# Kernel optimization log

Measured on AMD Instinct MI355X. Metric: run time of the kernel, lower is better.

The kernel has to match this reference:

```python
import jax, jax.numpy as jnp
import numpy as np

N, L, S, D, H, DK = 4, 2048, 2048, 1024, 16, 64


def setup_inputs() -> dict:
    key = jax.random.key(0)
    kq, kk, kv, kwq, kwo = jax.random.split(key, 5)
    Q = jax.random.normal(kq, (N, L, D), dtype=jnp.float32)
    K = jax.random.normal(kk, (N, S, D), dtype=jnp.float32)
    V = jax.random.normal(kv, (N, S, D), dtype=jnp.float32)
    # per-head query projection weights (the source reuses Lq for K and V too)
    Wq = jax.random.normal(kwq, (H, DK, D), dtype=jnp.float32) * (D ** -0.5)
    # output projection Lo: Linear(h*dv -> Dv), weight shape (out, in)
    Wo = jax.random.normal(kwo, (D, H * DK), dtype=jnp.float32) * ((H * DK) ** -0.5)
    return {"Q": Q, "K": K, "V": V, "Wq": Wq, "Wo": Wo}


def reference(Q, K, V, Wq, Wo):
    dk = Wq.shape[1]
    # Faithful to source: ALL of q, k, v are projected with the Lq weights.
    q = jnp.einsum('nld,hkd->hnlk', Q, Wq)   # (H,N,L,dk)
    k = jnp.einsum('nsd,hkd->hnsk', K, Wq)   # (H,N,S,dk)
    v = jnp.einsum('nsd,hkd->hnsk', V, Wq)   # (H,N,S,dk)
    scale = jnp.asarray(dk, Q.dtype) ** 0.5
    scores = jnp.einsum('hnlk,hnsk->hnls', q, k) / scale  # (H,N,L,S)
    # Faithful to F.softmax(dot) with no dim on a 3D tensor: torch picks dim=0
    # (the batch axis N); here that is axis=1 of the head-stacked (H,N,L,S).
    attn = jax.nn.softmax(scores, axis=1)
    heads = jnp.einsum('hnls,hnsk->hnlk', attn, v)        # (H,N,L,dk)
    # concat heads along last dim -> (N,L,H*dk)
    heads = jnp.transpose(heads, (1, 2, 0, 3)).reshape(Q.shape[0], Q.shape[1], -1)
    return heads @ Wo.T  # (N,L,Dv)
```

## Files before the change

kernel.cpp:

```cpp
#include <hip/hip_runtime.h>
#include <hip/hip_bf16.h>

typedef __attribute__((ext_vector_type(8))) short short8;
typedef __attribute__((ext_vector_type(4))) short short4v;
typedef __attribute__((ext_vector_type(4))) float float4v;

#define DEVI static __device__ __forceinline__

#if __has_builtin(__builtin_amdgcn_exp2f)
#define EXP2(x) __builtin_amdgcn_exp2f(x)
#else
#define EXP2(x) exp2f(x)
#endif

DEVI unsigned short f2bf(float f) {
  unsigned int u = __builtin_bit_cast(unsigned int, f);
  u += 0x7fffu + ((u >> 16) & 1u);
  return (unsigned short)(u >> 16);
}

DEVI short8 pack8(float4v a, float4v b) {
  struct P4 { __hip_bfloat162 x, y, z, w; } t;
  t.x = __float22bfloat162_rn(make_float2(a[0], a[1]));
  t.y = __float22bfloat162_rn(make_float2(a[2], a[3]));
  t.z = __float22bfloat162_rn(make_float2(b[0], b[1]));
  t.w = __float22bfloat162_rn(make_float2(b[2], b[3]));
  short8 r;
  __builtin_memcpy(&r, &t, 16);
  return r;
}

DEVI short4v pack4(float a, float b, float c, float d) {
  struct P2 { __hip_bfloat162 x, y; } t;
  t.x = __float22bfloat162_rn(make_float2(a, b));
  t.y = __float22bfloat162_rn(make_float2(c, d));
  short4v r;
  __builtin_memcpy(&r, &t, 8);
  return r;
}

DEVI void gload16(const void* src, void* lds_dst) {
  __builtin_amdgcn_global_load_lds(
      (const __attribute__((address_space(1))) void*)src,
      (__attribute__((address_space(3))) void*)lds_dst, 16, 0, 0);
}

__global__ __launch_bounds__(256)
void cvt_bf16(const float* __restrict__ in, unsigned short* __restrict__ out, int n8)
{
  int i = blockIdx.x * 256 + threadIdx.x;
  if (i < n8) {
    float4v a = *(const float4v*)(in + (size_t)i * 8);
    float4v b = *(const float4v*)(in + (size_t)i * 8 + 4);
    *(short8*)(out + (size_t)i * 8) = pack8(a, b);
  }
}

template<int AF32, int CMODE>
__global__ __launch_bounds__(256, 2)
void gemm_bt128(const void* __restrict__ Ap, const unsigned short* __restrict__ Bp,
                void* __restrict__ Cp, int M, int Nc, int Kd, float oscale)
{
  constexpr int AS = AF32 ? 40 : 32;
  __shared__ alignas(16) short As[2][128 * AS];
  __shared__ alignas(16) short Bs[2][128 * 32];

  const int tid = threadIdx.x;
  const int lane = tid & 63;
  const int wid = tid >> 6;
  const int rl = lane & 15;
  const int g = lane >> 4;
  const int bm = blockIdx.x * 128;
  const int bn = blockIdx.y * 128;
  const int wm = (wid >> 1) * 64;
  const int wn = (wid & 1) * 64;
  const int srow = tid >> 1;
  const int k0 = (tid & 1) * 16;

  float4v acc[4][4];
#pragma unroll
  for (int i = 0; i < 4; ++i)
#pragma unroll
    for (int j = 0; j < 4; ++j) acc[i][j] = (float4v)(0.0f);

  const float* Af = (const float*)Ap;
  const unsigned short* Ab = (const unsigned short*)Ap;

  float4v afr[4];
  short8 ah[2];

  const int NK = Kd >> 5;

  const int grow = (tid >> 2) + 0;
  const int gchk = tid & 3;

  auto stageB = [&](int ks, int b) {
#pragma unroll
    for (int j = 0; j < 2; ++j) {
      const unsigned short* src = Bp + (size_t)(bn + grow + j * 64) * Kd + ks * 32 + gchk * 8;
      gload16(src, (char*)Bs[b] + j * 4096 + wid * 1024);
    }
  };
  auto stageA16 = [&](int ks, int b) {
#pragma unroll
    for (int j = 0; j < 2; ++j) {
      const unsigned short* src = Ab + (size_t)(bm + grow + j * 64) * Kd + ks * 32 + gchk * 8;
      gload16(src, (char*)As[b] + j * 4096 + wid * 1024);
    }
  };
  auto loadA = [&](int ks) {
    size_t base = (size_t)(bm + srow) * Kd + ks * 32 + k0;
    afr[0] = *(const float4v*)(Af + base);
    afr[1] = *(const float4v*)(Af + base + 4);
    afr[2] = *(const float4v*)(Af + base + 8);
    afr[3] = *(const float4v*)(Af + base + 12);
  };
  auto packWriteA = [&](int b) {
    ah[0] = pack8(afr[0], afr[1]);
    ah[1] = pack8(afr[2], afr[3]);
    *(short8*)(As[b] + srow * 40 + k0)     = ah[0];
    *(short8*)(As[b] + srow * 40 + k0 + 8) = ah[1];
  };

  stageB(0, 0);
  if constexpr (AF32 != 0) {
    loadA(0);
    packWriteA(0);
  } else {
    stageA16(0, 0);
  }
  __syncthreads();

  for (int ks = 0; ks < NK; ++ks) {
    const int b = ks & 1;
    if (ks + 1 < NK) {
      stageB(ks + 1, b ^ 1);
      if constexpr (AF32 != 0) loadA(ks + 1);
      else stageA16(ks + 1, b ^ 1);
    }

    short8 a8[4], b8[4];
#pragma unroll
    for (int mt = 0; mt < 4; ++mt)
      a8[mt] = *(const short8*)(As[b] + (wm + mt * 16 + rl) * AS + 8 * g);
#pragma unroll
    for (int nt = 0; nt < 4; ++nt)
      b8[nt] = *(const short8*)(Bs[b] + (wn + nt * 16 + rl) * 32 + 8 * g);
#pragma unroll
    for (int mt = 0; mt < 4; ++mt)
#pragma unroll
      for (int nt = 0; nt < 4; ++nt)
        acc[mt][nt] = __builtin_amdgcn_mfma_f32_16x16x32_bf16(a8[mt], b8[nt], acc[mt][nt], 0, 0, 0);

    if constexpr (AF32 != 0)
      if (ks + 1 < NK) packWriteA(b ^ 1);
    __syncthreads();
  }

#pragma unroll
  for (int mt = 0; mt < 4; ++mt)
#pragma unroll
    for (int nt = 0; nt < 4; ++nt) {
      const int col = bn + wn + nt * 16 + rl;
      const int row0 = bm + wm + mt * 16 + 4 * g;
      if constexpr (CMODE == 1) {
        float* C = (float*)Cp;
#pragma unroll
        for (int r = 0; r < 4; ++r)
          C[(size_t)(row0 + r) * Nc + col] = acc[mt][nt][r];
      } else if constexpr (CMODE == 0) {
        unsigned short* C = (unsigned short*)Cp;
#pragma unroll
        for (int r = 0; r < 4; ++r)
          C[(size_t)(row0 + r) * Nc + col] = f2bf(acc[mt][nt][r] * oscale);
      } else {
        unsigned short* C = (unsigned short*)Cp;
        short4v w = pack4(acc[mt][nt][0], acc[mt][nt][1], acc[mt][nt][2], acc[mt][nt][3]);
        const int u = row0 & 31;
        const int pm = (row0 & ~31) | (((u >> 2) & 3) << 3) | (((u >> 4) & 1) << 2);
        *(short4v*)(C + (size_t)col * M + pm) = w;
      }
    }
}

__global__ __launch_bounds__(512, 2)
void attn_bn(const unsigned short* __restrict__ qb,
             const unsigned short* __restrict__ kb,
             const unsigned short* __restrict__ vtb,
             unsigned short* __restrict__ hb)
{
  __shared__ alignas(128) char smem[131072];

  const int tid = threadIdx.x;
  const int lane = tid & 63;
  const int wid = tid >> 6;
  const int rl = lane & 15;
  const int g = lane >> 4;
  const int h = blockIdx.y;
  const int l0 = blockIdx.x * 128 + wid * 16;

  short8 qf[4][2];
#pragma unroll
  for (int n = 0; n < 4; ++n)
#pragma unroll
    for (int dh = 0; dh < 2; ++dh)
      qf[n][dh] = *(const short8*)(qb + (size_t)(n * 2048 + l0 + rl) * 1024 + h * 64 + dh * 32 + 8 * g);

  float4v ha[4][4];
#pragma unroll
  for (int n = 0; n < 4; ++n)
#pragma unroll
    for (int t = 0; t < 4; ++t) ha[n][t] = (float4v)(0.0f);

  const size_t koff0 = ((size_t)(wid * 2048) + (size_t)(lane >> 3)) * 1024
                     + (size_t)(h * 64) + (size_t)(((lane & 7) ^ (lane >> 3)) * 8);
  const size_t voff0 = ((size_t)(h * 64) + (size_t)(lane >> 2)) * 8192
                     + (size_t)((wid - 4) * 2048)
                     + (size_t)((((lane & 3) ^ ((lane >> 3) & 3)) * 8));

  auto stage = [&](int step, int b) {
    if (wid < 4) {
      char* kdst = smem + b * 32768 + wid * 4096;
      const unsigned short* ksrc = kb + koff0 + (size_t)step * 32 * 1024;
#pragma unroll
      for (int ii = 0; ii < 4; ++ii)
        gload16(ksrc + ii * 8192, kdst + ii * 1024);
    } else {
      char* vdst = smem + b * 32768 + 16384 + (wid - 4) * 4096;
      const unsigned short* vsrc = vtb + voff0 + (size_t)step * 32;
#pragma unroll
      for (int ii = 0; ii < 4; ++ii)
        gload16(vsrc + (size_t)ii * 16 * 8192, vdst + ii * 1024);
    }
  };

  stage(0, 0);
  stage(1, 1);
  stage(2, 2);
  asm volatile("s_waitcnt vmcnt(8)" ::: "memory");
  __builtin_amdgcn_s_barrier();

  const unsigned voffr = ((unsigned)(g ^ ((rl >> 1) & 3))) << 4;

  for (int to = 0; to < 16; ++to) {
#pragma unroll
    for (int ti = 0; ti < 4; ++ti) {
      const int t = to * 4 + ti;
      char* kbase = smem + ti * 32768;
      char* vbase = kbase + 16384;

      float4v sc[4][2];
#pragma unroll
      for (int n = 0; n < 4; ++n) {
        char* kn = kbase + n * 4096;
#pragma unroll
        for (int ss = 0; ss < 2; ++ss) {
          const int srw = ss * 16 + rl;
          const unsigned sw = ((unsigned)(srw & 7)) << 4;
          short8 kf0 = *(const short8*)(kn + srw * 128 + ((16u * (unsigned)g) ^ sw));
          short8 kf1 = *(const short8*)(kn + srw * 128 + ((64u + 16u * (unsigned)g) ^ sw));
          float4v c = (float4v)(0.0f);
          c = __builtin_amdgcn_mfma_f32_16x16x32_bf16(kf0, qf[n][0], c, 0, 0, 0);
          c = __builtin_amdgcn_mfma_f32_16x16x32_bf16(kf1, qf[n][1], c, 0, 0, 0);
          sc[n][ss] = c;
        }
      }

      float ex[4][2][4];
#pragma unroll
      for (int ss = 0; ss < 2; ++ss) {
#pragma unroll
        for (int n = 0; n < 4; ++n)
#pragma unroll
          for (int r = 0; r < 4; ++r)
            ex[n][ss][r] = EXP2(sc[n][ss][r]);
#pragma unroll
        for (int r = 0; r < 4; ++r) {
          float inv = __builtin_amdgcn_rcpf((ex[0][ss][r] + ex[1][ss][r])
                                          + (ex[2][ss][r] + ex[3][ss][r]) + 1e-30f);
          ex[0][ss][r] *= inv; ex[1][ss][r] *= inv;
          ex[2][ss][r] *= inv; ex[3][ss][r] *= inv;
        }
      }
      short8 pf8[4];
#pragma unroll
      for (int n = 0; n < 4; ++n) {
        float4v e0 = {ex[n][0][0], ex[n][0][1], ex[n][0][2], ex[n][0][3]};
        float4v e1 = {ex[n][1][0], ex[n][1][1], ex[n][1][2], ex[n][1][3]};
        pf8[n] = pack8(e0, e1);
      }

#pragma unroll
      for (int n = 0; n < 4; ++n) {
        char* vn = vbase + n * 4096;
#pragma unroll
        for (int t4 = 0; t4 < 4; ++t4) {
          short8 va = *(const short8*)(vn + (t4 * 16 + rl) * 64 + voffr);
          ha[n][t4] = __builtin_amdgcn_mfma_f32_16x16x32_bf16(va, pf8[n], ha[n][t4], 0, 0, 0);
        }
      }

      if (t + 3 < 64) stage(t + 3, (ti + 3) & 3);
      asm volatile("s_waitcnt vmcnt(8)" ::: "memory");
      __builtin_amdgcn_s_barrier();
    }
  }

#pragma unroll
  for (int n = 0; n < 4; ++n)
#pragma unroll
    for (int tt = 0; tt < 4; ++tt) {
      short4v w = pack4(ha[n][tt][0], ha[n][tt][1], ha[n][tt][2], ha[n][tt][3]);
      size_t off = (size_t)(n * 2048 + l0 + rl) * 1024 + h * 64 + tt * 16 + 4 * g;
      *(short4v*)(hb + off) = w;
    }
}

extern "C" void kernel_launch(void* const* d_in, const int* in_sizes, int n_in,
                              void* d_out, int out_size, void* d_ws, size_t ws_size,
                              hipStream_t stream)
{
  const float* Q  = (const float*)d_in[0];
  const float* K  = (const float*)d_in[1];
  const float* V  = (const float*)d_in[2];
  const float* Wq = (const float*)d_in[3];
  const float* Wo = (const float*)d_in[4];

  unsigned short* qb  = (unsigned short*)d_ws;
  unsigned short* kw  = qb + (size_t)8192 * 1024;
  unsigned short* vt  = kw + (size_t)8192 * 1024;
  unsigned short* wqb = vt + (size_t)8192 * 1024;
  unsigned short* wob = wqb + (size_t)1024 * 1024;
  unsigned short* hw  = qb;

  const float CS = 0.18033688011112042f;

  dim3 gg(64, 8), bb(256);
  cvt_bf16<<<512, 256, 0, stream>>>(Wq, wqb, 131072);
  cvt_bf16<<<512, 256, 0, stream>>>(Wo, wob, 131072);
  gemm_bt128<1, 0><<<gg, bb, 0, stream>>>(Q, wqb, qb, 8192, 1024, 1024, CS);
  gemm_bt128<1, 0><<<gg, bb, 0, stream>>>(K, wqb, kw, 8192, 1024, 1024, 1.0f);
  gemm_bt128<1, 2><<<gg, bb, 0, stream>>>(V, wqb, vt, 8192, 1024, 1024, 1.0f);
  attn_bn<<<dim3(16, 16), dim3(512), 0, stream>>>(qb, kw, vt, hw);
  gemm_bt128<0, 1><<<gg, bb, 0, stream>>>(hw, wob, (float*)d_out, 8192, 1024, 1024, 1.0f);
}
```

Baseline: 239.2 us.

## Split batch axis across wave pairs, exchanging partial softmax sums via LDS

Each wave now handles two batch slices and 32 query rows instead of all four batch slices and 16 rows. Each K and V fragment loaded from LDS is therefore reused across two query tiles, which roughly halves LDS reads per MFMA. Because the softmax runs over the batch axis, paired waves exchange their partial exponent sums through an extra 16KB LDS buffer, synchronised with an added barrier each step. The exchanged sums are rounded to bf16, which costs some accuracy, and the larger LDS footprint may limit occupancy.

After: 249.1 us. +4.2%, slower.

```diff
diff --git a/kernel.cpp b/kernel.cpp
--- a/kernel.cpp
+++ b/kernel.cpp
@@ -17,6 +17,10 @@
   unsigned int u = __builtin_bit_cast(unsigned int, f);
   u += 0x7fffu + ((u >> 16) & 1u);
   return (unsigned short)(u >> 16);
+}
+
+DEVI float bf2f(unsigned short s) {
+  return __builtin_bit_cast(float, ((unsigned)s) << 16);
 }
 
 DEVI short8 pack8(float4v a, float4v b) {
@@ -91,7 +95,7 @@
 
   const int NK = Kd >> 5;
 
-  const int grow = (tid >> 2) + 0;
+  const int grow = tid >> 2;
   const int gchk = tid & 3;
 
   auto stageB = [&](int ks, int b) {
@@ -189,7 +193,7 @@
              const unsigned short* __restrict__ vtb,
              unsigned short* __restrict__ hb)
 {
-  __shared__ alignas(128) char smem[131072];
+  __shared__ alignas(128) char smem[147456];
 
   const int tid = threadIdx.x;
   const int lane = tid & 63;
@@ -197,20 +201,28 @@
   const int rl = lane & 15;
   const int g = lane >> 4;
   const int h = blockIdx.y;
-  const int l0 = blockIdx.x * 128 + wid * 16;
-
-  short8 qf[4][2];
-#pragma unroll
-  for (int n = 0; n < 4; ++n)
-#pragma unroll
-    for (int dh = 0; dh < 2; ++dh)
-      qf[n][dh] = *(const short8*)(qb + (size_t)(n * 2048 + l0 + rl) * 1024 + h * 64 + dh * 32 + 8 * g);
-
-  float4v ha[4][4];
-#pragma unroll
-  for (int n = 0; n < 4; ++n)
-#pragma unroll
-    for (int t = 0; t < 4; ++t) ha[n][t] = (float4v)(0.0f);
+  const int lg = wid & 3;
+  const int nh = wid >> 2;
+  const int n0 = nh * 2;
+  const int l0 = blockIdx.x * 128 + lg * 32;
+
+  short8 qf[2][2][2];
+#pragma unroll
+  for (int j = 0; j < 2; ++j)
+#pragma unroll
+    for (int lt = 0; lt < 2; ++lt)
+#pragma unroll
+      for (int dh = 0; dh < 2; ++dh)
+        qf[j][lt][dh] = *(const short8*)(qb
+            + (size_t)((n0 + j) * 2048 + l0 + lt * 16 + rl) * 1024 + h * 64 + dh * 32 + 8 * g);
+
+  float4v ha[2][2][4];
+#pragma unroll
+  for (int j = 0; j < 2; ++j)
+#pragma unroll
+    for (int lt = 0; lt < 2; ++lt)
+#pragma unroll
+      for (int t = 0; t < 4; ++t) ha[j][lt][t] = (float4v)(0.0f);
 
   const size_t koff0 = ((size_t)(wid * 2048) + (size_t)(lane >> 3)) * 1024
                      + (size_t)(h * 64) + (size_t)(((lane & 7) ^ (lane >> 3)) * 8);
@@ -241,6 +253,8 @@
   __builtin_amdgcn_s_barrier();
 
   const unsigned voffr = ((unsigned)(g ^ ((rl >> 1) & 3))) << 4;
+  char* exW = smem + 131072 + wid * 2048 + lane * 32;
+  char* exR = smem + 131072 + (wid ^ 4) * 2048 + lane * 32;
 
   for (int to = 0; to < 16; ++to) {
 #pragma unroll
@@ -249,54 +263,76 @@
       char* kbase = smem + ti * 32768;
       char* vbase = kbase + 16384;
 
-      float4v sc[4][2];
-#pragma unroll
-      for (int n = 0; n < 4; ++n) {
-        char* kn = kbase + n * 4096;
+      float4v sc[2][2][2];
+#pragma unroll
+      for (int j = 0; j < 2; ++j) {
+        char* kn = kbase + (n0 + j) * 4096;
 #pragma unroll
         for (int ss = 0; ss < 2; ++ss) {
           const int srw = ss * 16 + rl;
           const unsigned sw = ((unsigned)(srw & 7)) << 4;
           short8 kf0 = *(const short8*)(kn + srw * 128 + ((16u * (unsigned)g) ^ sw));
           short8 kf1 = *(const short8*)(kn + srw * 128 + ((64u + 16u * (unsigned)g) ^ sw));
-          float4v c = (float4v)(0.0f);
-          c = __builtin_amdgcn_mfma_f32_16x16x32_bf16(kf0, qf[n][0], c, 0, 0, 0);
-          c = __builtin_amdgcn_mfma_f32_16x16x32_bf16(kf1, qf[n][1], c, 0, 0, 0);
-          sc[n][ss] = c;
-        }
-      }
-
-      float ex[4][2][4];
-#pragma unroll
-      for (int ss = 0; ss < 2; ++ss) {
-#pragma unroll
-        for (int n = 0; n < 4; ++n)
+#pragma unroll
+          for (int lt = 0; lt < 2; ++lt) {
+            float4v c = (float4v)(0.0f);
+            c = __builtin_amdgcn_mfma_f32_16x16x32_bf16(kf0, qf[j][lt][0], c, 0, 0, 0);
+            c = __builtin_amdgcn_mfma_f32_16x16x32_bf16(kf1, qf[j][lt][1], c, 0, 0, 0);
+            sc[j][lt][ss] = c;
+          }
+        }
+      }
+
+      float ex[2][2][2][4];
+      float4v ps[2][2];
+#pragma unroll
+      for (int lt = 0; lt < 2; ++lt)
+#pragma unroll
+        for (int ss = 0; ss < 2; ++ss) {
+#pragma unroll
+          for (int j = 0; j < 2; ++j)
+#pragma unroll
+            for (int r = 0; r < 4; ++r)
+              ex[j][lt][ss][r] = EXP2(sc[j][lt][ss][r]);
 #pragma unroll
           for (int r = 0; r < 4; ++r)
-            ex[n][ss][r] = EXP2(sc[n][ss][r]);
-#pragma unroll
-        for (int r = 0; r < 4; ++r) {
-          float inv = __builtin_amdgcn_rcpf((ex[0][ss][r] + ex[1][ss][r])
-                                          + (ex[2][ss][r] + ex[3][ss][r]) + 1e-30f);
-          ex[0][ss][r] *= inv; ex[1][ss][r] *= inv;
-          ex[2][ss][r] *= inv; ex[3][ss][r] *= inv;
-        }
-      }
-      short8 pf8[4];
-#pragma unroll
-      for (int n = 0; n < 4; ++n) {
-        float4v e0 = {ex[n][0][0], ex[n][0][1], ex[n][0][2], ex[n][0][3]};
-        float4v e1 = {ex[n][1][0], ex[n][1][1], ex[n][1][2], ex[n][1][3]};
-        pf8[n] = pack8(e0, e1);
-      }
-
-#pragma unroll
-      for (int n = 0; n < 4; ++n) {
-        char* vn = vbase + n * 4096;
+            ps[lt][ss][r] = ex[0][lt][ss][r] + ex[1][lt][ss][r];
+          *(short4v*)(exW + (lt * 2 + ss) * 8) =
+              pack4(ps[lt][ss][0], ps[lt][ss][1], ps[lt][ss][2], ps[lt][ss][3]);
+        }
+      __builtin_amdgcn_s_barrier();
+
+      short8 pf8[2][2];
+#pragma unroll
+      for (int lt = 0; lt < 2; ++lt) {
+#pragma unroll
+        for (int ss = 0; ss < 2; ++ss) {
+          short4v po = *(const short4v*)(exR + (lt * 2 + ss) * 8);
+#pragma unroll
+          for (int r = 0; r < 4; ++r) {
+            float inv = __builtin_amdgcn_rcpf(
+                ps[lt][ss][r] + bf2f((unsigned short)po[r]) + 1e-30f);
+            ex[0][lt][ss][r] *= inv;
+            ex[1][lt][ss][r] *= inv;
+          }
+        }
+#pragma unroll
+        for (int j = 0; j < 2; ++j) {
+          float4v e0 = {ex[j][lt][0][0], ex[j][lt][0][1], ex[j][lt][0][2], ex[j][lt][0][3]};
+          float4v e1 = {ex[j][lt][1][0], ex[j][lt][1][1], ex[j][lt][1][2], ex[j][lt][1][3]};
+          pf8[j][lt] = pack8(e0, e1);
+        }
+      }
+
+#pragma unroll
+      for (int j = 0; j < 2; ++j) {
+        char* vn = vbase + (n0 + j) * 4096;
 #pragma unroll
         for (int t4 = 0; t4 < 4; ++t4) {
           short8 va = *(const short8*)(vn + (t4 * 16 + rl) * 64 + voffr);
-          ha[n][t4] = __builtin_amdgcn_mfma_f32_16x16x32_bf16(va, pf8[n], ha[n][t4], 0, 0, 0);
+#pragma unroll
+          for (int lt = 0; lt < 2; ++lt)
+            ha[j][lt][t4] = __builtin_amdgcn_mfma_f32_16x16x32_bf16(va, pf8[j][lt], ha[j][lt][t4], 0, 0, 0);
         }
       }
 
@@ -307,13 +343,16 @@
   }
 
 #pragma unroll
-  for (int n = 0; n < 4; ++n)
-#pragma unroll
-    for (int tt = 0; tt < 4; ++tt) {
-      short4v w = pack4(ha[n][tt][0], ha[n][tt][1], ha[n][tt][2], ha[n][tt][3]);
-      size_t off = (size_t)(n * 2048 + l0 + rl) * 1024 + h * 64 + tt * 16 + 4 * g;
-      *(short4v*)(hb + off) = w;
-    }
+  for (int j = 0; j < 2; ++j)
+#pragma unroll
+    for (int lt = 0; lt < 2; ++lt)
+#pragma unroll
+      for (int tt = 0; tt < 4; ++tt) {
+        short4v w = pack4(ha[j][lt][tt][0], ha[j][lt][tt][1], ha[j][lt][tt][2], ha[j][lt][tt][3]);
+        size_t off = (size_t)((n0 + j) * 2048 + l0 + lt * 16 + rl) * 1024
+                   + h * 64 + tt * 16 + 4 * g;
+        *(short4v*)(hb + off) = w;
+      }
 }
 
 extern "C" void kernel_launch(void* const* d_in, const int* in_sizes, int n_in,
```
